# Kernel optimization log

Hardware: AMD Instinct MI355X
Metric: run time of the kernel (lower is better)

The kernel has to match this reference:

```python
import jax, jax.numpy as jnp
import numpy as np


def _chamfer_one(x, y):
    # x: [N,3], y: [M,3]; squared-Euclidean pairwise distances via norm expansion
    x2 = jnp.sum(x * x, axis=-1)  # [N]
    y2 = jnp.sum(y * y, axis=-1)  # [M]
    cross = jnp.einsum('nd,md->nm', x, y)  # [N,M]
    d = x2[:, None] + y2[None, :] - 2.0 * cross  # [N,M] squared distances
    # kaolin chamfer_distance: mean of NN sq-dists in both directions, summed (w1=w2=1)
    return jnp.mean(jnp.min(d, axis=1)) + jnp.mean(jnp.min(d, axis=0))


def reference(x, y):
    # x, y: [B, N, 3] / [B, M, 3]
    per_sample = jax.vmap(_chamfer_one)(x, y)  # [B]
    return jnp.mean(per_sample)


def setup_inputs() -> dict:
    key = jax.random.key(0)
    kx, ky = jax.random.split(key)
    x = jax.random.normal(kx, (16, 4096, 3), dtype=jnp.float32)
    y = jax.random.normal(ky, (16, 4096, 3), dtype=jnp.float32)
    return {"x": x, "y": y}
```

## Files before the change

kernel.cpp:

```cpp
#include <hip/hip_runtime.h>
#include <hip/hip_fp16.h>
#include <math.h>


typedef _Float16 f16x8  __attribute__((ext_vector_type(8)));
typedef float    f32x16 __attribute__((ext_vector_type(16)));

constexpr int BATCH  = 16;
constexpr int NPTS   = 4096;
constexpr int NDB    = 2 * BATCH;
constexpr int BLOCK  = 256;
constexpr int QPB    = 256;
constexpr int CHUNK  = 2048;
constexpr int NCHUNK = NPTS / CHUNK;
constexpr int NBLK   = NDB * (NPTS / QPB);

__device__ __forceinline__ void cvt_point(float a, float b, float c,
                                          _Float16& ha, _Float16& hb,
                                          _Float16& hc, _Float16& shi,
                                          _Float16& slo) {
    ha = (_Float16)a; hb = (_Float16)b; hc = (_Float16)c;
    float fa = (float)ha, fb = (float)hb, fc = (float)hc;
    float ss = fa * fa + fb * fb + fc * fc;
    shi = (_Float16)ss;
    slo = (_Float16)(ss - (float)shi);
}

__device__ __forceinline__ f16x8 make_afrag(const float* __restrict__ Gb,
                                            int j) {
    const _Float16 one = (_Float16)1.0f, zz = (_Float16)0.0f;
    _Float16 ha, hb, hc, shi, slo;
    cvt_point(Gb[3 * j], Gb[3 * j + 1], Gb[3 * j + 2], ha, hb, hc, shi, slo);
    return (f16x8){ (_Float16)(-2.0f * (float)ha),
                    (_Float16)(-2.0f * (float)hb),
                    (_Float16)(-2.0f * (float)hc),
                    shi, slo, one, one, zz };
}

__global__ void __launch_bounds__(BLOCK, 2)
chamfer_fused(const float* __restrict__ x, const float* __restrict__ y,
              float* __restrict__ out) {
    const int bid   = blockIdx.x;
    const int qgrp  = bid & 15;
    const int db    = bid >> 4;
    const int dir   = db >> 4;
    const int batch = db & (BATCH - 1);
    const int lane  = threadIdx.x & 63;
    const int wave  = threadIdx.x >> 6;
    const int m     = lane & 31;

    const float* P  = dir ? y : x;
    const float* G  = dir ? x : y;
    const float* Pb = P + (size_t)batch * NPTS * 3;
    const float* Gb = G + (size_t)batch * NPTS * 3;

    const _Float16 one = (_Float16)1.0f, zz = (_Float16)0.0f;

    f16x8 bfrag0, bfrag1;
    {
        int qi0 = qgrp * QPB + (wave * 2 + 0) * 32 + m;
        int qi1 = qgrp * QPB + (wave * 2 + 1) * 32 + m;
        _Float16 ha, hb, hc, shi, slo;
        cvt_point(Pb[3 * qi0], Pb[3 * qi0 + 1], Pb[3 * qi0 + 2],
                  ha, hb, hc, shi, slo);
        bfrag0 = (f16x8){ ha, hb, hc, one, one, shi, slo, zz };
        cvt_point(Pb[3 * qi1], Pb[3 * qi1 + 1], Pb[3 * qi1 + 2],
                  ha, hb, hc, shi, slo);
        bfrag1 = (f16x8){ ha, hb, hc, one, one, shi, slo, zz };
    }

    __shared__ f16x8 As[2][CHUNK];

    #pragma unroll
    for (int r = 0; r < CHUNK / BLOCK; ++r)
        As[0][r * BLOCK + threadIdx.x] = make_afrag(Gb, r * BLOCK + threadIdx.x);

    const f32x16 z = {0.0f, 0.0f, 0.0f, 0.0f, 0.0f, 0.0f, 0.0f, 0.0f,
                      0.0f, 0.0f, 0.0f, 0.0f, 0.0f, 0.0f, 0.0f, 0.0f};
    float a00 = INFINITY, a01 = INFINITY;
    float a10 = INFINITY, a11 = INFINITY;

    for (int ch = 0; ch < NCHUNK; ++ch) {
        __syncthreads();
        const int cur = ch & 1;
        if (ch + 1 < NCHUNK) {
            #pragma unroll
            for (int r = 0; r < CHUNK / BLOCK; ++r) {
                int s = r * BLOCK + threadIdx.x;
                As[cur ^ 1][s] = make_afrag(Gb, (ch + 1) * CHUNK + s);
            }
        }
        #pragma unroll 4
        for (int tt = 0; tt < CHUNK / 32; ++tt) {
            f16x8 af = As[cur][tt * 32 + m];
            f32x16 d0 = __builtin_amdgcn_mfma_f32_32x32x16_f16(af, bfrag0, z,
                                                               0, 0, 0);
            f32x16 d1 = __builtin_amdgcn_mfma_f32_32x32x16_f16(af, bfrag1, z,
                                                               0, 0, 0);
            a00 = fminf(fminf(d0[0],  d0[1]),  a00);
            a01 = fminf(fminf(d0[8],  d0[9]),  a01);
            a10 = fminf(fminf(d1[0],  d1[1]),  a10);
            a11 = fminf(fminf(d1[8],  d1[9]),  a11);
            a00 = fminf(fminf(d0[2],  d0[3]),  a00);
            a01 = fminf(fminf(d0[10], d0[11]), a01);
            a10 = fminf(fminf(d1[2],  d1[3]),  a10);
            a11 = fminf(fminf(d1[10], d1[11]), a11);
            a00 = fminf(fminf(d0[4],  d0[5]),  a00);
            a01 = fminf(fminf(d0[12], d0[13]), a01);
            a10 = fminf(fminf(d1[4],  d1[5]),  a10);
            a11 = fminf(fminf(d1[12], d1[13]), a11);
            a00 = fminf(fminf(d0[6],  d0[7]),  a00);
            a01 = fminf(fminf(d0[14], d0[15]), a01);
            a10 = fminf(fminf(d1[6],  d1[7]),  a10);
            a11 = fminf(fminf(d1[14], d1[15]), a11);
        }
    }
    float acc0 = fminf(a00, a01);
    float acc1 = fminf(a10, a11);

    acc0 = fminf(acc0, __shfl_xor(acc0, 32, 64));
    acc1 = fminf(acc1, __shfl_xor(acc1, 32, 64));
    float acc = acc0 + acc1;
    #pragma unroll
    for (int off = 1; off < 64; off <<= 1) acc += __shfl_xor(acc, off, 64);

    __shared__ float s4[4];
    if (lane == 0) s4[wave] = acc;
    __syncthreads();
    if (threadIdx.x == 0) {
        float b = (s4[0] + s4[1]) + (s4[2] + s4[3]);
        atomicAdd(out, b * (0.25f / ((float)BATCH * (float)NPTS)));
    }
}

extern "C" void kernel_launch(void* const* d_in, const int* in_sizes, int n_in,
                              void* d_out, int out_size, void* d_ws, size_t ws_size,
                              hipStream_t stream) {
    const float* x = (const float*)d_in[0];
    const float* y = (const float*)d_in[1];
    float* out = (float*)d_out;

    hipLaunchKernelGGL(chamfer_fused, dim3(NBLK), dim3(BLOCK), 0, stream,
                       x, y, out);
}
```

Baseline: 72.52 us.

## Stage full target set in LDS, split across 8 waves, software-pipeline MFMA

Blocks grow to 512 threads and load all 4096 target fragments into LDS once, replacing the double-buffered chunk loop and its per-chunk barriers. Waves are split into two halves that each scan half of the targets. The inner loop overlaps the next MFMA pair with the min-folding of the previous results. The two halves' per-query minima are then combined through LDS before the final sum and atomic add. In exchange the block uses 64 KB of LDS, which limits how many blocks fit per CU, and the final reduction adds extra barriers.

```diff
diff --git a/kernel.cpp b/kernel.cpp
--- a/kernel.cpp
+++ b/kernel.cpp
@@ -6,14 +6,14 @@
 typedef _Float16 f16x8  __attribute__((ext_vector_type(8)));
 typedef float    f32x16 __attribute__((ext_vector_type(16)));
 
-constexpr int BATCH  = 16;
-constexpr int NPTS   = 4096;
-constexpr int NDB    = 2 * BATCH;
-constexpr int BLOCK  = 256;
-constexpr int QPB    = 256;
-constexpr int CHUNK  = 2048;
-constexpr int NCHUNK = NPTS / CHUNK;
-constexpr int NBLK   = NDB * (NPTS / QPB);
+constexpr int BATCH = 16;
+constexpr int NPTS  = 4096;
+constexpr int NDB   = 2 * BATCH;
+constexpr int BLOCK = 512;
+constexpr int QPB   = 256;
+constexpr int NBLK  = NDB * (NPTS / QPB);
+constexpr int THALF = NPTS / 2;
+constexpr int ITERS = THALF / 32;
 
 __device__ __forceinline__ void cvt_point(float a, float b, float c,
                                           _Float16& ha, _Float16& hb,
@@ -37,7 +37,18 @@
                     shi, slo, one, one, zz };
 }
 
-__global__ void __launch_bounds__(BLOCK, 2)
+__device__ __forceinline__ void fold16(const f32x16& d, float& A0, float& A1) {
+    A0 = fminf(fminf(d[0],  d[1]),  A0);
+    A0 = fminf(fminf(d[2],  d[3]),  A0);
+    A0 = fminf(fminf(d[4],  d[5]),  A0);
+    A0 = fminf(fminf(d[6],  d[7]),  A0);
+    A1 = fminf(fminf(d[8],  d[9]),  A1);
+    A1 = fminf(fminf(d[10], d[11]), A1);
+    A1 = fminf(fminf(d[12], d[13]), A1);
+    A1 = fminf(fminf(d[14], d[15]), A1);
+}
+
+__global__ void __launch_bounds__(BLOCK, 4)
 chamfer_fused(const float* __restrict__ x, const float* __restrict__ y,
               float* __restrict__ out) {
     const int bid   = blockIdx.x;
@@ -48,6 +59,8 @@
     const int lane  = threadIdx.x & 63;
     const int wave  = threadIdx.x >> 6;
     const int m     = lane & 31;
+    const int tpair = wave & 3;
+    const int half  = wave >> 2;
 
     const float* P  = dir ? y : x;
     const float* G  = dir ? x : y;
@@ -58,78 +71,81 @@
 
     f16x8 bfrag0, bfrag1;
     {
-        int qi0 = qgrp * QPB + (wave * 2 + 0) * 32 + m;
-        int qi1 = qgrp * QPB + (wave * 2 + 1) * 32 + m;
+        int q0 = qgrp * QPB + (tpair * 2 + 0) * 32 + m;
+        int q1 = q0 + 32;
         _Float16 ha, hb, hc, shi, slo;
-        cvt_point(Pb[3 * qi0], Pb[3 * qi0 + 1], Pb[3 * qi0 + 2],
+        cvt_point(Pb[3 * q0], Pb[3 * q0 + 1], Pb[3 * q0 + 2],
                   ha, hb, hc, shi, slo);
         bfrag0 = (f16x8){ ha, hb, hc, one, one, shi, slo, zz };
-        cvt_point(Pb[3 * qi1], Pb[3 * qi1 + 1], Pb[3 * qi1 + 2],
+        cvt_point(Pb[3 * q1], Pb[3 * q1 + 1], Pb[3 * q1 + 2],
                   ha, hb, hc, shi, slo);
         bfrag1 = (f16x8){ ha, hb, hc, one, one, shi, slo, zz };
     }
 
-    __shared__ f16x8 As[2][CHUNK];
+    __shared__ f16x8 As[NPTS];
 
     #pragma unroll
-    for (int r = 0; r < CHUNK / BLOCK; ++r)
-        As[0][r * BLOCK + threadIdx.x] = make_afrag(Gb, r * BLOCK + threadIdx.x);
+    for (int r = 0; r < NPTS / BLOCK; ++r) {
+        int s = r * BLOCK + threadIdx.x;
+        As[s] = make_afrag(Gb, s);
+    }
+    __syncthreads();
 
     const f32x16 z = {0.0f, 0.0f, 0.0f, 0.0f, 0.0f, 0.0f, 0.0f, 0.0f,
                       0.0f, 0.0f, 0.0f, 0.0f, 0.0f, 0.0f, 0.0f, 0.0f};
     float a00 = INFINITY, a01 = INFINITY;
     float a10 = INFINITY, a11 = INFINITY;
 
-    for (int ch = 0; ch < NCHUNK; ++ch) {
-        __syncthreads();
-        const int cur = ch & 1;
-        if (ch + 1 < NCHUNK) {
-            #pragma unroll
-            for (int r = 0; r < CHUNK / BLOCK; ++r) {
-                int s = r * BLOCK + threadIdx.x;
-                As[cur ^ 1][s] = make_afrag(Gb, (ch + 1) * CHUNK + s);
-            }
-        }
-        #pragma unroll 4
-        for (int tt = 0; tt < CHUNK / 32; ++tt) {
-            f16x8 af = As[cur][tt * 32 + m];
-            f32x16 d0 = __builtin_amdgcn_mfma_f32_32x32x16_f16(af, bfrag0, z,
-                                                               0, 0, 0);
-            f32x16 d1 = __builtin_amdgcn_mfma_f32_32x32x16_f16(af, bfrag1, z,
-                                                               0, 0, 0);
-            a00 = fminf(fminf(d0[0],  d0[1]),  a00);
-            a01 = fminf(fminf(d0[8],  d0[9]),  a01);
-            a10 = fminf(fminf(d1[0],  d1[1]),  a10);
-            a11 = fminf(fminf(d1[8],  d1[9]),  a11);
-            a00 = fminf(fminf(d0[2],  d0[3]),  a00);
-            a01 = fminf(fminf(d0[10], d0[11]), a01);
-            a10 = fminf(fminf(d1[2],  d1[3]),  a10);
-            a11 = fminf(fminf(d1[10], d1[11]), a11);
-            a00 = fminf(fminf(d0[4],  d0[5]),  a00);
-            a01 = fminf(fminf(d0[12], d0[13]), a01);
-            a10 = fminf(fminf(d1[4],  d1[5]),  a10);
-            a11 = fminf(fminf(d1[12], d1[13]), a11);
-            a00 = fminf(fminf(d0[6],  d0[7]),  a00);
-            a01 = fminf(fminf(d0[14], d0[15]), a01);
-            a10 = fminf(fminf(d1[6],  d1[7]),  a10);
-            a11 = fminf(fminf(d1[14], d1[15]), a11);
-        }
+    const f16x8* Ab = As + half * THALF + m;
+    f16x8 af0 = Ab[0];
+    f32x16 dA0 = __builtin_amdgcn_mfma_f32_32x32x16_f16(af0, bfrag0, z, 0, 0, 0);
+    f32x16 dA1 = __builtin_amdgcn_mfma_f32_32x32x16_f16(af0, bfrag1, z, 0, 0, 0);
+    f16x8 afB = Ab[32];
+    #pragma unroll 2
+    for (int tt = 1; tt < ITERS - 1; ++tt) {
+        f16x8 afC = Ab[(tt + 1) * 32];
+        f32x16 dB0 = __builtin_amdgcn_mfma_f32_32x32x16_f16(afB, bfrag0, z, 0, 0, 0);
+        f32x16 dB1 = __builtin_amdgcn_mfma_f32_32x32x16_f16(afB, bfrag1, z, 0, 0, 0);
+        fold16(dA0, a00, a01);
+        fold16(dA1, a10, a11);
+        dA0 = dB0; dA1 = dB1; afB = afC;
     }
+    {
+        f32x16 dB0 = __builtin_amdgcn_mfma_f32_32x32x16_f16(afB, bfrag0, z, 0, 0, 0);
+        f32x16 dB1 = __builtin_amdgcn_mfma_f32_32x32x16_f16(afB, bfrag1, z, 0, 0, 0);
+        fold16(dA0, a00, a01);
+        fold16(dA1, a10, a11);
+        fold16(dB0, a00, a01);
+        fold16(dB1, a10, a11);
+    }
+
     float acc0 = fminf(a00, a01);
     float acc1 = fminf(a10, a11);
-
     acc0 = fminf(acc0, __shfl_xor(acc0, 32, 64));
     acc1 = fminf(acc1, __shfl_xor(acc1, 32, 64));
-    float acc = acc0 + acc1;
-    #pragma unroll
-    for (int off = 1; off < 64; off <<= 1) acc += __shfl_xor(acc, off, 64);
 
-    __shared__ float s4[4];
-    if (lane == 0) s4[wave] = acc;
+    __syncthreads();
+    float* sred = reinterpret_cast<float*>(As);
+    if (lane < 32) {
+        sred[(wave * 2 + 0) * 32 + m] = acc0;
+        sred[(wave * 2 + 1) * 32 + m] = acc1;
+    }
+    __syncthreads();
+    if (threadIdx.x < 256) {
+        const int tile = threadIdx.x >> 5;
+        const int col  = threadIdx.x & 31;
+        const int wl   = tile >> 1;
+        const int slot = tile & 1;
+        float v = fminf(sred[(wl * 2 + slot) * 32 + col],
+                        sred[((wl + 4) * 2 + slot) * 32 + col]);
+        #pragma unroll
+        for (int off = 1; off < 64; off <<= 1) v += __shfl_xor(v, off, 64);
+        if ((threadIdx.x & 63) == 0) sred[512 + (threadIdx.x >> 6)] = v;
+    }
     __syncthreads();
     if (threadIdx.x == 0) {
-        float b = (s4[0] + s4[1]) + (s4[2] + s4[3]);
-        atomicAdd(out, b * (0.25f / ((float)BATCH * (float)NPTS)));
+        float b = (sred[512] + sred[513]) + (sred[514] + sred[515]);
+        atomicAdd(out, b * (0.5f / ((float)BATCH * (float)NPTS)));
     }
 }
 
```

Measured after the change: 73.55 us. Within noise of the previous version (+1.4%).
